# Kernel tuning notes

Hardware: AMD Instinct MI355X
Metric: run time of the kernel (lower is better)

Reference implementation:

```python
import jax, jax.numpy as jnp
import numpy as np

EPS = 1e-05
BITW = 8
BITA = 8


def _ste_round(v):
    # round with identity gradient (TF Round->Identity override)
    return v + jax.lax.stop_gradient(jnp.round(v) - v)


def _quantize_overflow(x, bits):
    # tensorlayer _quantize_overflow: linear quantization over [min, max]
    n = 2.0 ** bits - 1.0
    mx = jnp.max(x)
    mn = jnp.min(x)
    step = jax.lax.stop_gradient((mx - mn) / n)
    return _ste_round((x - mn) / step) * step + mn


def _conv2d_same(x, w):
    # x: [N,H,W,C], w: [KH,KW,C,F]
    return jax.lax.conv_general_dilated(
        x, w, window_strides=(1, 1), padding='SAME',
        dimension_numbers=('NHWC', 'HWIO', 'NHWC'))


def setup_inputs() -> dict:
    key = jax.random.key(0)
    k1, k2 = jax.random.split(key)
    x = jax.random.normal(k1, (32, 56, 56, 128), dtype=jnp.float32)
    W = jax.random.normal(k2, (3, 3, 128, 256), dtype=jnp.float32) * 0.02
    gamma = jnp.ones((256,), dtype=jnp.float32)
    beta = jnp.zeros((256,), dtype=jnp.float32)
    return {"x": x, "W": W, "gamma": gamma, "beta": beta}


def reference(x, W, gamma, beta):
    # 1) fake-quantize activations
    xq = _quantize_overflow(x, BITA)
    # 2) full-precision conv to get batch statistics (training path)
    conv_out = _conv2d_same(x, W)  # [N,H,W,F]
    mean = jnp.mean(conv_out, axis=(0, 1, 2))          # [F]
    var = jnp.var(conv_out, axis=(0, 1, 2))            # [F], biased (tf.nn.moments)
    inv_std = 1.0 / jnp.sqrt(var + EPS)                # [F]
    # 3) fold BN into weights/bias
    w_fold = W * (gamma * inv_std)                     # broadcast over [KH,KW,C,F]
    bias_fold = beta - gamma * mean * inv_std          # [F]
    # 4) quantize folded weights, conv with quantized activations
    wq = _quantize_overflow(w_fold, BITW)
    out = _conv2d_same(xq, wq) + bias_fold
    return jax.nn.relu(out)
```

## Files before the change

### kernel.cpp

```cpp
#include <hip/hip_runtime.h>

typedef float f32x4_t __attribute__((ext_vector_type(4)));
typedef __bf16 bf16x8_t __attribute__((ext_vector_type(8)));
typedef unsigned short u16x8_t __attribute__((ext_vector_type(8)));

#define NPIX        100352
#define PIX_PER_IMG 3136
#define PH          58
#define PPIX        3364
#define C_IN        128
#define C_OUT       256
#define NTAPS       9
#define NV4         3211264
#define NWELEM      294912
#define MTILES      392
#define NPADPIX     107648

#define OFF_ENC     0
#define OFF_SCALE   64
#define OFF_BIAS    1152
#define OFF_WT      4096
#define OFF_WQT     593920
#define OFF_PSUM    1183744
#define OFF_PSQ     1986560
#define OFF_XPAD    2789376
#define OFF_XQPAD   30347264

__device__ __forceinline__ unsigned short f2bf(float x) {
  unsigned u = __float_as_uint(x);
  u += 0x7FFFu + ((u >> 16) & 1u);
  return (unsigned short)(u >> 16);
}
__device__ __forceinline__ unsigned encf(float v) {
  unsigned u = __float_as_uint(v);
  return (u & 0x80000000u) ? ~u : (u | 0x80000000u);
}
__device__ __forceinline__ float decf(unsigned e) {
  unsigned u = (e & 0x80000000u) ? (e ^ 0x80000000u) : ~e;
  return __uint_as_float(u);
}
__device__ __forceinline__ void gl_lds16(const void* g, void* l) {
  auto gp = (const __attribute__((address_space(1))) unsigned*)(const unsigned*)g;
  auto lp = (__attribute__((address_space(3))) unsigned*)(unsigned*)l;
  __builtin_amdgcn_global_load_lds(gp, lp, 16, 0, 0);
}
#define SCHED_FENCE() __builtin_amdgcn_sched_barrier(0)

__global__ void kinit(unsigned* enc) {
  enc[0] = 0xFFFFFFFFu;
  enc[1] = 0u;
  enc[2] = 0xFFFFFFFFu;
  enc[3] = 0u;
}

__global__ void kminmax(const float4* __restrict__ x, unsigned* __restrict__ enc) {
  const int tid = blockIdx.x * blockDim.x + threadIdx.x;
  const int stride = gridDim.x * blockDim.x;
  float mn = 3.4e38f, mx = -3.4e38f;
  for (int i = tid; i < NV4; i += stride) {
    float4 v = x[i];
    mn = fminf(mn, fminf(fminf(v.x, v.y), fminf(v.z, v.w)));
    mx = fmaxf(mx, fmaxf(fmaxf(v.x, v.y), fmaxf(v.z, v.w)));
  }
  #pragma unroll
  for (int off = 32; off > 0; off >>= 1) {
    mn = fminf(mn, __shfl_xor(mn, off));
    mx = fmaxf(mx, __shfl_xor(mx, off));
  }
  __shared__ float smn[4], smx[4];
  const int lane = threadIdx.x & 63, w = threadIdx.x >> 6;
  if (lane == 0) { smn[w] = mn; smx[w] = mx; }
  __syncthreads();
  if (threadIdx.x == 0) {
    mn = fminf(fminf(smn[0], smn[1]), fminf(smn[2], smn[3]));
    mx = fmaxf(fmaxf(smx[0], smx[1]), fmaxf(smx[2], smx[3]));
    atomicMin(&enc[0], encf(mn));
    atomicMax(&enc[1], encf(mx));
  }
}

__global__ void kwconv(const float* __restrict__ W, unsigned short* __restrict__ wt) {
  const int idx = blockIdx.x * 256 + threadIdx.x;
  if (idx >= NWELEM) return;
  const int c = idx & 127;
  const int f = (idx >> 7) & 255;
  const int tap = idx >> 15;
  wt[idx] = f2bf(W[(tap * 128 + c) * 256 + f]);
}

__global__ void kwq(const float* __restrict__ W, const float* __restrict__ scale,
                    const unsigned* __restrict__ enc, unsigned short* __restrict__ wqt) {
  const int idx = blockIdx.x * 256 + threadIdx.x;
  if (idx >= NWELEM) return;
  const int c = idx & 127;
  const int f = (idx >> 7) & 255;
  const int tap = idx >> 15;
  const float wmn = decf(enc[2]), wmx = decf(enc[3]);
  const float wstep = (wmx - wmn) / 255.0f;
  const float wrstep = 255.0f / (wmx - wmn);
  const float v = W[(tap * 128 + c) * 256 + f] * scale[f];
  const float q = rintf((v - wmn) * wrstep) * wstep + wmn;
  wqt[idx] = f2bf(q);
}

__global__ void kpadfill(const float* __restrict__ x, const unsigned* __restrict__ enc,
                         unsigned short* __restrict__ xpad, unsigned short* __restrict__ xqpad)
{
  const int tid = blockIdx.x * 256 + threadIdx.x;
  if (tid >= NPADPIX * 16) return;
  const int pp = tid >> 4;
  const int c8 = (tid & 15) << 3;
  const int n = pp / PPIX;
  const int rem = pp - n * PPIX;
  const int hp = rem / PH;
  const int wp = rem - hp * PH;
  u16x8_t vb, vq;
  #pragma unroll
  for (int j = 0; j < 8; ++j) { vb[j] = 0; vq[j] = 0; }
  if (hp >= 1 && hp <= 56 && wp >= 1 && wp <= 56) {
    const float mn = decf(enc[0]), mx = decf(enc[1]);
    const float step = (mx - mn) / 255.0f, rstep = 255.0f / (mx - mn);
    const float* src = x + ((n * PIX_PER_IMG) + (hp - 1) * 56 + (wp - 1)) * C_IN + c8;
    const float4 a = *(const float4*)src;
    const float4 b = *(const float4*)(src + 4);
    const float v[8] = {a.x, a.y, a.z, a.w, b.x, b.y, b.z, b.w};
    #pragma unroll
    for (int j = 0; j < 8; ++j) {
      vb[j] = f2bf(v[j]);
      const float qv = rintf((v[j] - mn) * rstep) * step + mn;
      vq[j] = f2bf(qv);
    }
  }
  *(u16x8_t*)(xpad + pp * C_IN + c8) = vb;
  *(u16x8_t*)(xqpad + pp * C_IN + c8) = vq;
}

template<int STATS>
__global__ __launch_bounds__(512, 4)
void kconv(const unsigned short* __restrict__ xin,
           const unsigned short* __restrict__ wt,
           float* __restrict__ out,
           const float* __restrict__ bias,
           float* __restrict__ psum,
           float* __restrict__ psq)
{
  const int bid = blockIdx.x;
  const int slot = (bid & 7) * 98 + (bid >> 3);
  const int bm = slot >> 1;
  const int bn = slot & 1;

  const int tid = threadIdx.x;
  const int lane = tid & 63;
  const int wid = tid >> 6;
  const int wm = wid >> 1;
  const int wn = wid & 1;
  const int l16 = lane & 15;
  const int rsub = lane >> 4;

  __shared__ __align__(16) unsigned char smem[49152];

  unsigned aoff[2];
  {
    const int arow0 = wid * 8 + (lane >> 3);
    const int pc = lane & 7;
    #pragma unroll
    for (int j = 0; j < 2; ++j) {
      const int row = j * 64 + arow0;
      const int lc = pc ^ (row & 7);
      const int pix = bm * 256 + row + 128 * (lc >> 2);
      const int n = pix / PIX_PER_IMG;
      const int rem = pix - n * PIX_PER_IMG;
      const int hh = rem / 56;
      const int ww = rem - hh * 56;
      aoff[j] = (unsigned)((n * PPIX + hh * PH + ww) * C_IN + (lc & 3) * 8);
    }
  }
  unsigned boff;
  {
    const int row = wid * 8 + (lane >> 3);
    const int pc = lane & 7;
    const int lc = pc ^ (row & 7);
    const int f = bn * 128 + row + 64 * (lc >> 2);
    boff = (unsigned)(f * C_IN + (lc & 3) * 8);
  }

  int a_rd[4], b_rd[4];
  #pragma unroll
  for (int im = 0; im < 4; ++im) {
    const int p = wm * 64 + im * 16 + l16;
    const int row = p & 127, half = p >> 7;
    const int phys = (half * 4 + rsub) ^ (row & 7);
    a_rd[im] = row * 128 + phys * 16;
  }
  #pragma unroll
  for (int in = 0; in < 4; ++in) {
    const int f = wn * 64 + in * 16 + l16;
    const int row = f & 63, half = f >> 6;
    const int phys = (half * 4 + rsub) ^ (row & 7);
    b_rd[in] = row * 128 + phys * 16;
  }

  f32x4_t acc[4][4];
  #pragma unroll
  for (int im = 0; im < 4; ++im)
    #pragma unroll
    for (int in = 0; in < 4; ++in)
      #pragma unroll
      for (int j = 0; j < 4; ++j) acc[im][in][j] = 0.f;

  auto stage = [&](int s) {
    const int tap = s >> 2;
    const int cq = (s & 3) * 32;
    const int kh = tap / 3, kw = tap - kh * 3;
    const unsigned atap = (unsigned)((kh * PH + kw) * C_IN + cq);
    const unsigned btap = (unsigned)(tap * (C_OUT * C_IN) + cq);
    unsigned char* sA = smem + (s & 1) * 24576;
    unsigned char* sB = sA + 16384;
    gl_lds16(xin + atap + aoff[0], sA + wid * 1024);
    gl_lds16(xin + atap + aoff[1], sA + 8192 + wid * 1024);
    gl_lds16(wt + btap + boff, sB + wid * 1024);
  };

  auto compute = [&](int s) {
    const unsigned char* sA = smem + (s & 1) * 24576;
    const unsigned char* sB = sA + 16384;
    bf16x8_t av[4], bv[4];
    #pragma unroll
    for (int im = 0; im < 4; ++im)
      av[im] = *(const bf16x8_t*)(sA + a_rd[im]);
    #pragma unroll
    for (int in = 0; in < 4; ++in)
      bv[in] = *(const bf16x8_t*)(sB + b_rd[in]);
    #pragma unroll
    for (int im = 0; im < 4; ++im)
      #pragma unroll
      for (int in = 0; in < 4; ++in)
        acc[im][in] = __builtin_amdgcn_mfma_f32_16x16x32_bf16(av[im], bv[in], acc[im][in], 0, 0, 0);
  };

  stage(0);
  stage(1);

  #pragma unroll 1
  for (int s = 0; s < 35; ++s) {
    asm volatile("s_waitcnt vmcnt(3)" ::: "memory");
    SCHED_FENCE();
    __builtin_amdgcn_s_barrier();
    SCHED_FENCE();
    compute(s);
    SCHED_FENCE();
    __builtin_amdgcn_s_barrier();
    SCHED_FENCE();
    if (s < 34) stage(s + 2);
  }
  asm volatile("s_waitcnt vmcnt(0)" ::: "memory");
  SCHED_FENCE();
  __builtin_amdgcn_s_barrier();
  SCHED_FENCE();
  compute(35);

  if (STATS) {
    __syncthreads();
    float* sb = (float*)smem;
    #pragma unroll
    for (int in = 0; in < 4; ++in) {
      float s = 0.f, q = 0.f;
      #pragma unroll
      for (int im = 0; im < 4; ++im)
        #pragma unroll
        for (int j = 0; j < 4; ++j) {
          const float v = acc[im][in][j];
          s += v; q += v * v;
        }
      s += __shfl_xor(s, 16); q += __shfl_xor(q, 16);
      s += __shfl_xor(s, 32); q += __shfl_xor(q, 32);
      if (lane < 16) {
        sb[wid * 64 + in * 16 + lane] = s;
        sb[512 + wid * 64 + in * 16 + lane] = q;
      }
    }
    __syncthreads();
    if (tid < 128) {
      const int wn2 = tid >> 6, cl = tid & 63;
      float s = 0.f, q = 0.f;
      #pragma unroll
      for (int wm2 = 0; wm2 < 4; ++wm2) {
        s += sb[(wm2 * 2 + wn2) * 64 + cl];
        q += sb[512 + (wm2 * 2 + wn2) * 64 + cl];
      }
      psum[(bm * 2 + bn) * 128 + tid] = s;
      psq[(bm * 2 + bn) * 128 + tid] = q;
    }
  } else {
    float bval[4];
    #pragma unroll
    for (int in = 0; in < 4; ++in)
      bval[in] = bias[bn * 128 + wn * 64 + in * 16 + l16];
    #pragma unroll
    for (int im = 0; im < 4; ++im) {
      #pragma unroll
      for (int j = 0; j < 4; ++j) {
        const int pix = bm * 256 + wm * 64 + im * 16 + rsub * 4 + j;
        #pragma unroll
        for (int in = 0; in < 4; ++in) {
          const int f = bn * 128 + wn * 64 + in * 16 + l16;
          out[pix * 256 + f] = fmaxf(acc[im][in][j] + bval[in], 0.f);
        }
      }
    }
  }
}

__global__ __launch_bounds__(256)
void kstats(const float* __restrict__ psum, const float* __restrict__ psq,
            const float* __restrict__ gamma, const float* __restrict__ beta,
            float* __restrict__ scale, float* __restrict__ bias)
{
  const int ch = blockIdx.x;
  const int bn = ch >> 7, col = ch & 127;
  float s = 0.f, q = 0.f;
  for (int bm = threadIdx.x; bm < MTILES; bm += 256) {
    s += psum[(bm * 2 + bn) * 128 + col];
    q += psq[(bm * 2 + bn) * 128 + col];
  }
  #pragma unroll
  for (int off = 32; off > 0; off >>= 1) {
    s += __shfl_xor(s, off);
    q += __shfl_xor(q, off);
  }
  __shared__ float ss[4], sq2[4];
  const int lane = threadIdx.x & 63, w = threadIdx.x >> 6;
  if (lane == 0) { ss[w] = s; sq2[w] = q; }
  __syncthreads();
  if (threadIdx.x == 0) {
    s = ss[0] + ss[1] + ss[2] + ss[3];
    q = sq2[0] + sq2[1] + sq2[2] + sq2[3];
    const float inv = 1.0f / (float)NPIX;
    const float mean = s * inv;
    const float var = q * inv - mean * mean;
    const float istd = 1.0f / sqrtf(var + 1e-5f);
    const float g = gamma[ch];
    scale[ch] = g * istd;
    bias[ch] = beta[ch] - g * mean * istd;
  }
}

__global__ __launch_bounds__(256)
void kwmm(const float* __restrict__ W, const float* __restrict__ scale,
          unsigned* __restrict__ enc)
{
  const int idx = blockIdx.x * 256 + threadIdx.x;
  float v = 0.f;
  if (idx < NWELEM) v = W[idx] * scale[idx & 255];
  float mn = v, mx = v;
  #pragma unroll
  for (int off = 32; off > 0; off >>= 1) {
    mn = fminf(mn, __shfl_xor(mn, off));
    mx = fmaxf(mx, __shfl_xor(mx, off));
  }
  __shared__ float rmn[4], rmx[4];
  const int lane = threadIdx.x & 63, w = threadIdx.x >> 6;
  if (lane == 0) { rmn[w] = mn; rmx[w] = mx; }
  __syncthreads();
  if (threadIdx.x == 0) {
    mn = fminf(fminf(rmn[0], rmn[1]), fminf(rmn[2], rmn[3]));
    mx = fmaxf(fmaxf(rmx[0], rmx[1]), fmaxf(rmx[2], rmx[3]));
    atomicMin(&enc[2], encf(mn));
    atomicMax(&enc[3], encf(mx));
  }
}

extern "C" void kernel_launch(void* const* d_in, const int* in_sizes, int n_in,
                              void* d_out, int out_size, void* d_ws, size_t ws_size,
                              hipStream_t stream)
{
  const float* x     = (const float*)d_in[0];
  const float* W     = (const float*)d_in[1];
  const float* gamma = (const float*)d_in[2];
  const float* beta  = (const float*)d_in[3];
  float* out = (float*)d_out;
  char* ws = (char*)d_ws;

  unsigned* enc        = (unsigned*)(ws + OFF_ENC);
  float* scale         = (float*)(ws + OFF_SCALE);
  float* bias          = (float*)(ws + OFF_BIAS);
  unsigned short* Wt   = (unsigned short*)(ws + OFF_WT);
  unsigned short* Wqt  = (unsigned short*)(ws + OFF_WQT);
  float* psum          = (float*)(ws + OFF_PSUM);
  float* psq           = (float*)(ws + OFF_PSQ);
  unsigned short* xpad  = (unsigned short*)(ws + OFF_XPAD);
  unsigned short* xqpad = (unsigned short*)(ws + OFF_XQPAD);

  kinit<<<1, 64, 0, stream>>>(enc);
  kminmax<<<1024, 256, 0, stream>>>((const float4*)x, enc);
  kwconv<<<1152, 256, 0, stream>>>(W, Wt);
  kpadfill<<<6728, 256, 0, stream>>>(x, enc, xpad, xqpad);
  kconv<1><<<784, 512, 0, stream>>>(xpad, Wt, nullptr, nullptr, psum, psq);
  kstats<<<256, 256, 0, stream>>>(psum, psq, gamma, beta, scale, bias);
  kwmm<<<1152, 256, 0, stream>>>(W, scale, enc);
  kwq<<<1152, 256, 0, stream>>>(W, scale, enc, Wqt);
  kconv<0><<<784, 512, 0, stream>>>(xqpad, Wqt, out, bias, nullptr, nullptr);
}
```

Measured before the change: 236.7 us.

## Fold weight-convert and per-channel weight min/max into padfill, drop kwmm

The weight bf16 conversion kernel is merged into the padfill launch as extra blocks. New blocks compute the per-output-channel min and max of the raw weights. Because the folded weight is W times a per-channel scale, kstats now derives the global min/max of the folded weights from those per-channel extremes times the scale, which removes the separate kwmm pass over all weights. This cuts two launches and a full weight read, at the cost of strided column reads in the new min/max blocks.

```diff
diff --git a/kernel.cpp b/kernel.cpp
--- a/kernel.cpp
+++ b/kernel.cpp
@@ -10,7 +10,6 @@
 #define PPIX        3364
 #define C_IN        128
 #define C_OUT       256
-#define NTAPS       9
 #define NV4         3211264
 #define NWELEM      294912
 #define MTILES      392
@@ -22,6 +21,8 @@
 #define OFF_WT      4096
 #define OFF_WQT     593920
 #define OFF_PSUM    1183744
+#define OFF_WFMIN   1585152
+#define OFF_WFMAX   1586176
 #define OFF_PSQ     1986560
 #define OFF_XPAD    2789376
 #define OFF_XQPAD   30347264
@@ -47,10 +48,8 @@
 #define SCHED_FENCE() __builtin_amdgcn_sched_barrier(0)
 
 __global__ void kinit(unsigned* enc) {
-  enc[0] = 0xFFFFFFFFu;
-  enc[1] = 0u;
-  enc[2] = 0xFFFFFFFFu;
-  enc[3] = 0u;
+  enc[0] = 0xFFFFFFFFu; enc[1] = 0u;
+  enc[2] = 0xFFFFFFFFu; enc[3] = 0u;
 }
 
 __global__ void kminmax(const float4* __restrict__ x, unsigned* __restrict__ enc) {
@@ -77,15 +76,6 @@
     atomicMin(&enc[0], encf(mn));
     atomicMax(&enc[1], encf(mx));
   }
-}
-
-__global__ void kwconv(const float* __restrict__ W, unsigned short* __restrict__ wt) {
-  const int idx = blockIdx.x * 256 + threadIdx.x;
-  if (idx >= NWELEM) return;
-  const int c = idx & 127;
-  const int f = (idx >> 7) & 255;
-  const int tap = idx >> 15;
-  wt[idx] = f2bf(W[(tap * 128 + c) * 256 + f]);
 }
 
 __global__ void kwq(const float* __restrict__ W, const float* __restrict__ scale,
@@ -104,8 +94,42 @@
 }
 
 __global__ void kpadfill(const float* __restrict__ x, const unsigned* __restrict__ enc,
-                         unsigned short* __restrict__ xpad, unsigned short* __restrict__ xqpad)
+                         unsigned short* __restrict__ xpad, unsigned short* __restrict__ xqpad,
+                         const float* __restrict__ W, unsigned short* __restrict__ wtt,
+                         float* __restrict__ wfmin, float* __restrict__ wfmax)
 {
+  if (blockIdx.x >= 7880) {
+    const int f = blockIdx.x - 7880;
+    float mn = 3.4e38f, mx = -3.4e38f;
+    for (int e = threadIdx.x; e < 1152; e += 256) {
+      const float v = W[e * 256 + f];
+      mn = fminf(mn, v); mx = fmaxf(mx, v);
+    }
+    #pragma unroll
+    for (int off = 32; off > 0; off >>= 1) {
+      mn = fminf(mn, __shfl_xor(mn, off));
+      mx = fmaxf(mx, __shfl_xor(mx, off));
+    }
+    __shared__ float rmn[4], rmx[4];
+    const int lane = threadIdx.x & 63, w = threadIdx.x >> 6;
+    if (lane == 0) { rmn[w] = mn; rmx[w] = mx; }
+    __syncthreads();
+    if (threadIdx.x == 0) {
+      wfmin[f] = fminf(fminf(rmn[0], rmn[1]), fminf(rmn[2], rmn[3]));
+      wfmax[f] = fmaxf(fmaxf(rmx[0], rmx[1]), fmaxf(rmx[2], rmx[3]));
+    }
+    return;
+  }
+  if (blockIdx.x >= 6728) {
+    const int idx = (blockIdx.x - 6728) * 256 + threadIdx.x;
+    if (idx < NWELEM) {
+      const int c = idx & 127;
+      const int f = (idx >> 7) & 255;
+      const int tap = idx >> 15;
+      wtt[idx] = f2bf(W[(tap * 128 + c) * 256 + f]);
+    }
+    return;
+  }
   const int tid = blockIdx.x * 256 + threadIdx.x;
   if (tid >= NPADPIX * 16) return;
   const int pp = tid >> 4;
@@ -226,11 +250,9 @@
     const unsigned char* sB = sA + 16384;
     bf16x8_t av[4], bv[4];
     #pragma unroll
-    for (int im = 0; im < 4; ++im)
-      av[im] = *(const bf16x8_t*)(sA + a_rd[im]);
-    #pragma unroll
-    for (int in = 0; in < 4; ++in)
-      bv[in] = *(const bf16x8_t*)(sB + b_rd[in]);
+    for (int im = 0; im < 4; ++im) av[im] = *(const bf16x8_t*)(sA + a_rd[im]);
+    #pragma unroll
+    for (int in = 0; in < 4; ++in) bv[in] = *(const bf16x8_t*)(sB + b_rd[in]);
     #pragma unroll
     for (int im = 0; im < 4; ++im)
       #pragma unroll
@@ -314,7 +336,9 @@
 __global__ __launch_bounds__(256)
 void kstats(const float* __restrict__ psum, const float* __restrict__ psq,
             const float* __restrict__ gamma, const float* __restrict__ beta,
-            float* __restrict__ scale, float* __restrict__ bias)
+            float* __restrict__ scale, float* __restrict__ bias,
+            const float* __restrict__ wfmin, const float* __restrict__ wfmax,
+            unsigned* __restrict__ enc)
 {
   const int ch = blockIdx.x;
   const int bn = ch >> 7, col = ch & 127;
@@ -340,33 +364,13 @@
     const float var = q * inv - mean * mean;
     const float istd = 1.0f / sqrtf(var + 1e-5f);
     const float g = gamma[ch];
-    scale[ch] = g * istd;
+    const float sc = g * istd;
+    scale[ch] = sc;
     bias[ch] = beta[ch] - g * mean * istd;
-  }
-}
-
-__global__ __launch_bounds__(256)
-void kwmm(const float* __restrict__ W, const float* __restrict__ scale,
-          unsigned* __restrict__ enc)
-{
-  const int idx = blockIdx.x * 256 + threadIdx.x;
-  float v = 0.f;
-  if (idx < NWELEM) v = W[idx] * scale[idx & 255];
-  float mn = v, mx = v;
-  #pragma unroll
-  for (int off = 32; off > 0; off >>= 1) {
-    mn = fminf(mn, __shfl_xor(mn, off));
-    mx = fmaxf(mx, __shfl_xor(mx, off));
-  }
-  __shared__ float rmn[4], rmx[4];
-  const int lane = threadIdx.x & 63, w = threadIdx.x >> 6;
-  if (lane == 0) { rmn[w] = mn; rmx[w] = mx; }
-  __syncthreads();
-  if (threadIdx.x == 0) {
-    mn = fminf(fminf(rmn[0], rmn[1]), fminf(rmn[2], rmn[3]));
-    mx = fmaxf(fmaxf(rmx[0], rmx[1]), fmaxf(rmx[2], rmx[3]));
-    atomicMin(&enc[2], encf(mn));
-    atomicMax(&enc[3], encf(mx));
+    const float p0 = sc * wfmin[ch];
+    const float p1 = sc * wfmax[ch];
+    atomicMin(&enc[2], encf(fminf(p0, p1)));
+    atomicMax(&enc[3], encf(fmaxf(p0, p1)));
   }
 }
 
@@ -387,17 +391,17 @@
   unsigned short* Wt   = (unsigned short*)(ws + OFF_WT);
   unsigned short* Wqt  = (unsigned short*)(ws + OFF_WQT);
   float* psum          = (float*)(ws + OFF_PSUM);
+  float* wfmin         = (float*)(ws + OFF_WFMIN);
+  float* wfmax         = (float*)(ws + OFF_WFMAX);
   float* psq           = (float*)(ws + OFF_PSQ);
   unsigned short* xpad  = (unsigned short*)(ws + OFF_XPAD);
   unsigned short* xqpad = (unsigned short*)(ws + OFF_XQPAD);
 
   kinit<<<1, 64, 0, stream>>>(enc);
   kminmax<<<1024, 256, 0, stream>>>((const float4*)x, enc);
-  kwconv<<<1152, 256, 0, stream>>>(W, Wt);
-  kpadfill<<<6728, 256, 0, stream>>>(x, enc, xpad, xqpad);
+  kpadfill<<<8136, 256, 0, stream>>>(x, enc, xpad, xqpad, W, Wt, wfmin, wfmax);
   kconv<1><<<784, 512, 0, stream>>>(xpad, Wt, nullptr, nullptr, psum, psq);
-  kstats<<<256, 256, 0, stream>>>(psum, psq, gamma, beta, scale, bias);
-  kwmm<<<1152, 256, 0, stream>>>(W, scale, enc);
+  kstats<<<256, 256, 0, stream>>>(psum, psq, gamma, beta, scale, bias, wfmin, wfmax, enc);
   kwq<<<1152, 256, 0, stream>>>(W, scale, enc, Wqt);
   kconv<0><<<784, 512, 0, stream>>>(xqpad, Wqt, out, bias, nullptr, nullptr);
 }
```

Result: faster. 215.5 us (median of 3 runs) (-9.0%).
